# Kernel tuning notes

Hardware: AMD Instinct MI355X
Metric: run time of the kernel (lower is better)

The kernel has to match this reference:

```python
import jax, jax.numpy as jnp
import numpy as np

D_MODEL = 256
N_HEADS = 8


def setup_inputs() -> dict:
    key = jax.random.key(0)
    ks = jax.random.split(key, 12)
    B, S, d, H = 4, 1024, D_MODEL, N_HEADS
    s = 0.02
    return {
        "Q": jax.random.normal(ks[0], (B, S, d), jnp.float32),
        "K": jax.random.normal(ks[1], (B, S, d), jnp.float32),
        "V": jax.random.normal(ks[2], (B, S, d), jnp.float32),
        "Wq": jax.random.normal(ks[3], (d, d * H), jnp.float32) * s,
        "bq": jnp.zeros((d * H,), jnp.float32),
        "Wk": jax.random.normal(ks[4], (d, d * H), jnp.float32) * s,
        "bk": jnp.zeros((d * H,), jnp.float32),
        "Wv": jax.random.normal(ks[5], (d, d * H), jnp.float32) * s,
        "bv": jnp.zeros((d * H,), jnp.float32),
        "Wo": jax.random.normal(ks[6], (H * d, d), jnp.float32) * s,
        "bo": jnp.zeros((d,), jnp.float32),
    }


def reference(Q, K, V, Wq, bq, Wk, bk, Wv, bv, Wo, bo):
    B, S, d = Q.shape
    H = N_HEADS
    # projections: [B,S,d] -> [B,S,H*d] -> [B,H,S,d] (head_dim == d_model here)
    q = (Q @ Wq + bq).reshape(B, S, H, d).transpose(0, 2, 1, 3)
    k = (K @ Wk + bk).reshape(B, S, H, d).transpose(0, 2, 1, 3)
    v = (V @ Wv + bv).reshape(B, S, H, d).transpose(0, 2, 1, 3)
    scores = jnp.einsum("bhqd,bhkd->bhqk", q, k) / jnp.sqrt(jnp.float32(d))
    attn = jax.nn.softmax(scores, axis=-1)
    out = jnp.einsum("bhqk,bhkd->bhqd", attn, v)  # [B,H,S,d]
    out = out.transpose(0, 2, 1, 3).reshape(B, S, H * d)
    return out @ Wo + bo
```

## Files before the change

### kernel.cpp

```cpp
#include <hip/hip_runtime.h>
#include <stdint.h>

#define NB 4
#define SEQ 1024
#define DM 256
#define NH 8

typedef __attribute__((ext_vector_type(8))) short bf8;
typedef __attribute__((ext_vector_type(4))) float f4;

__device__ __forceinline__ unsigned short f2bf(float f) {
  union { float f; uint32_t u; } c; c.f = f;
  uint32_t u = c.u;
  return (unsigned short)((u + 0x7FFFu + ((u >> 16) & 1u)) >> 16);
}

__device__ __forceinline__ float bf2f(short s) {
  union { uint32_t u; float f; } c;
  c.u = ((uint32_t)(unsigned short)s) << 16;
  return c.f;
}

__device__ __forceinline__ void gl_lds16(const unsigned short* g, short* l) {
  __builtin_amdgcn_global_load_lds(
      (const __attribute__((address_space(1))) unsigned int*)g,
      (__attribute__((address_space(3))) unsigned int*)l, 16, 0, 0);
}


__global__ __launch_bounds__(256) void prep_kernel(
    const float* __restrict__ Wq, const float* __restrict__ Wk,
    const float* __restrict__ Wv, const float* __restrict__ Wo,
    const float* __restrict__ Q, const float* __restrict__ K,
    const float* __restrict__ V,
    unsigned short* __restrict__ Wt3, unsigned short* __restrict__ WoT,
    unsigned short* __restrict__ Xbf) {
  const int z = blockIdx.y;
  const int tid = threadIdx.x;
  if (z >= 4) {
    const float* src = (z == 4) ? Q : (z == 5) ? K : V;
    const size_t off = (size_t)blockIdx.x * 1024 + tid * 4;
    const float4 v = *(const float4*)(src + off);
    short4 s;
    s.x = (short)f2bf(v.x); s.y = (short)f2bf(v.y);
    s.z = (short)f2bf(v.z); s.w = (short)f2bf(v.w);
    *(short4*)(Xbf + (size_t)(z - 4) * 4096 * 256 + off) = s;
    return;
  }
  if (blockIdx.x >= 512) return;
  const float* in;
  unsigned short* out;
  int R, C, bx, by;
  if (z < 3) {
    in = (z == 0) ? Wq : (z == 1) ? Wk : Wv;
    out = Wt3 + (size_t)z * 2048 * 256;
    R = 256; C = 2048; bx = blockIdx.x & 63; by = blockIdx.x >> 6;
  } else {
    in = Wo; out = WoT;
    R = 2048; C = 256; bx = blockIdx.x & 7; by = blockIdx.x >> 3;
  }
  __shared__ float t[32][33];
  const int c0 = bx * 32, r0 = by * 32;
  const int tx = tid & 31, ty = tid >> 5;
#pragma unroll
  for (int i = 0; i < 4; i++) {
    int r = r0 + ty + i * 8;
    t[ty + i * 8][tx] = in[(size_t)r * C + c0 + tx];
  }
  __syncthreads();
#pragma unroll
  for (int i = 0; i < 4; i++) {
    int c = c0 + ty + i * 8;
    out[(size_t)c * R + r0 + tx] = f2bf(t[tx][ty + i * 8]);
  }
}

__global__ __launch_bounds__(256) void proj_kernel(
    const unsigned short* __restrict__ Xbf, const unsigned short* __restrict__ Wt3,
    const float* __restrict__ bq, const float* __restrict__ bk, const float* __restrict__ bv,
    unsigned short* __restrict__ q_frag, unsigned short* __restrict__ k_frag,
    unsigned short* __restrict__ v_frag) {
  const int z = blockIdx.z;
  const unsigned short* X = Xbf + (size_t)z * 4096 * 256;
  const unsigned short* Wt = Wt3 + (size_t)z * 2048 * 256;
  const float* bias = (z == 0) ? bq : (z == 1) ? bk : bv;

  __shared__ short a_lds[128 * 32];
  __shared__ short b_lds[128 * 32];

  const int tid = threadIdx.x;
  const int wid = tid >> 6, lane = tid & 63;
  const int quad = lane >> 4, l16 = lane & 15;
  const int wm = wid >> 1, wn = wid & 1;
  const int m0 = blockIdx.x * 128, n0 = blockIdx.y * 128;

  f4 acc[4][4];
  const f4 z4 = {0.f, 0.f, 0.f, 0.f};
#pragma unroll
  for (int i = 0; i < 4; i++)
#pragma unroll
    for (int j = 0; j < 4; j++) acc[i][j] = z4;

  const int srow = lane >> 2;
  const int schunk = lane & 3;
  const int cxor = quad ^ (l16 & 3);

  for (int ko = 0; ko < 8; ko++) {
    const int k0 = ko * 32;
#pragma unroll
    for (int j = 0; j < 2; j++) {
      const int i = wid * 2 + j;
      const int row = i * 16 + srow;
      const int sc = (schunk ^ (row & 3)) * 8;
      gl_lds16(X + (size_t)(m0 + row) * DM + k0 + sc, a_lds + i * 512);
      gl_lds16(Wt + (size_t)(n0 + row) * DM + k0 + sc, b_lds + i * 512);
    }
    __syncthreads();
    bf8 af[4], bfv[4];
#pragma unroll
    for (int mi = 0; mi < 4; mi++)
      af[mi] = *(const bf8*)(a_lds + (wm * 64 + mi * 16 + l16) * 32 + cxor * 8);
#pragma unroll
    for (int ni = 0; ni < 4; ni++)
      bfv[ni] = *(const bf8*)(b_lds + (wn * 64 + ni * 16 + l16) * 32 + cxor * 8);
    if (z < 2) {
#pragma unroll
      for (int ni = 0; ni < 4; ni++)
#pragma unroll
        for (int mi = 0; mi < 4; mi++)
          acc[ni][mi] = __builtin_amdgcn_mfma_f32_16x16x32_bf16(bfv[ni], af[mi], acc[ni][mi], 0, 0, 0);
    } else {
#pragma unroll
      for (int mi = 0; mi < 4; mi++)
#pragma unroll
        for (int ni = 0; ni < 4; ni++)
          acc[mi][ni] = __builtin_amdgcn_mfma_f32_16x16x32_bf16(af[mi], bfv[ni], acc[mi][ni], 0, 0, 0);
    }
    __syncthreads();
  }

  if (z < 2) {
    const float scale = (z == 0) ? 0.0901684400f : 1.0f;
    unsigned short* dst = (z == 0) ? q_frag : k_frag;
#pragma unroll
    for (int ni = 0; ni < 4; ni++) {
      const int nb = n0 + wn * 64 + ni * 16 + quad * 4;
      const float4 b4 = *(const float4*)(bias + nb);
      const int h = nb >> 8, dd = nb & 255;
      const int dq = (dd >> 3) & 3, jh = dd & 7;
#pragma unroll
      for (int mi = 0; mi < 4; mi++) {
        const int tok = m0 + wm * 64 + mi * 16 + l16;
        const int b = tok >> 10, sr = tok & 1023;
        const size_t idx = ((size_t)(b * NH + h) * 64 + (sr >> 4)) * 4096 +
                           (size_t)(dd >> 5) * 512 + ((sr & 15) + 16 * dq) * 8 + jh;
        short4 s4;
        s4.x = (short)f2bf((acc[ni][mi][0] + b4.x) * scale);
        s4.y = (short)f2bf((acc[ni][mi][1] + b4.y) * scale);
        s4.z = (short)f2bf((acc[ni][mi][2] + b4.z) * scale);
        s4.w = (short)f2bf((acc[ni][mi][3] + b4.w) * scale);
        *(short4*)(dst + idx) = s4;
      }
    }
  } else {
#pragma unroll
    for (int ni = 0; ni < 4; ni++) {
      const int n = n0 + wn * 64 + ni * 16 + l16;
      const float bsv = bias[n];
      const int h = n >> 8, d = n & 255;
#pragma unroll
      for (int mi = 0; mi < 4; mi++) {
        const int m = m0 + wm * 64 + mi * 16 + quad * 4;
        const int b = m >> 10, sr = m & 1023;
        const size_t idx = ((size_t)(b * NH + h) * 16 + (d >> 4)) * 16384 +
                           (size_t)(sr >> 5) * 512 +
                           ((d & 15) + 16 * ((sr >> 3) & 3)) * 8 + (sr & 7);
        short4 s4;
        s4.x = (short)f2bf(acc[mi][ni][0] + bsv);
        s4.y = (short)f2bf(acc[mi][ni][1] + bsv);
        s4.z = (short)f2bf(acc[mi][ni][2] + bsv);
        s4.w = (short)f2bf(acc[mi][ni][3] + bsv);
        *(short4*)(v_frag + idx) = s4;
      }
    }
  }
}

__global__ __launch_bounds__(256, 3) void attn_kernel(
    const unsigned short* __restrict__ q_frag, const unsigned short* __restrict__ k_frag,
    const unsigned short* __restrict__ v_frag, unsigned short* __restrict__ o_p0,
    unsigned short* __restrict__ o_p1, float* __restrict__ l_part, const int split) {
  __shared__ short k_lds[2][8192];
  __shared__ short p_lds[2][64][40];

  const int tid = threadIdx.x;
  const int wid = tid >> 6, lane = tid & 63;
  const int quad = lane >> 4, l16 = lane & 15;
  const int blk = blockIdx.x;
  const int g = blk & 7;
  const int qt = (blk >> 3) & 15;
  const int kvh = split ? ((blk >> 7) & 1) : 0;
  const int bh = g + 8 * (blk >> (split ? 8 : 7));
  const int t0 = kvh * 16;
  const int tlast = t0 + (split ? 15 : 31);
  const int nhalf = split ? 8 : 16;
  const size_t fbase = (size_t)bh * 262144;

  bf8 qf[8];
  {
    const unsigned short* qp = q_frag + fbase + (size_t)(qt * 4 + wid) * 4096 + lane * 8;
#pragma unroll
    for (int kc = 0; kc < 8; kc++) qf[kc] = *(const bf8*)(qp + kc * 512);
  }

  const f4 z4 = {0.f, 0.f, 0.f, 0.f};
  f4 Oacc[4][4];
#pragma unroll
  for (int i = 0; i < 4; i++)
#pragma unroll
    for (int j = 0; j < 4; j++) Oacc[i][j] = z4;
  float lpart[4] = {0.f, 0.f, 0.f, 0.f};

  const unsigned short* kdma_src = k_frag + fbase + (size_t)wid * 2048 + lane * 8;
#pragma unroll
  for (int jj = 0; jj < 4; jj++)
    gl_lds16(kdma_src + (size_t)t0 * 8192 + jj * 512, &k_lds[0][wid * 2048 + jj * 512]);
  __syncthreads();

  bf8 vpre0[4], vpre1[4];
  const unsigned short* vbase_p = v_frag + fbase + (size_t)(wid * 4) * 16384 + lane * 8;

#define ATTN_STEP(T, CUR, PRV, VCUR, VPRV)                                     \
  {                                                                            \
    const int t_ = (T);                                                        \
    _Pragma("unroll")                                                          \
    for (int mi = 0; mi < 4; mi++)                                             \
      VCUR[mi] = *(const bf8*)(vbase_p + (size_t)mi * 16384 + (size_t)t_ * 512); \
    f4 Sacc[2];                                                                \
    Sacc[0] = z4; Sacc[1] = z4;                                                \
    _Pragma("unroll")                                                          \
    for (int kc = 0; kc < 8; kc++) {                                           \
      const bf8 aq = qf[kc];                                                   \
      _Pragma("unroll")                                                        \
      for (int ni = 0; ni < 2; ni++) {                                         \
        const bf8 kb = *(const bf8*)(&k_lds[CUR][(ni * 8 + kc) * 512 + lane * 8]); \
        Sacc[ni] = __builtin_amdgcn_mfma_f32_16x16x32_bf16(aq, kb, Sacc[ni], 0, 0, 0); \
      }                                                                        \
    }                                                                          \
    if (t_ < tlast) {                                                          \
      _Pragma("unroll")                                                        \
      for (int jj = 0; jj < 4; jj++)                                           \
        gl_lds16(kdma_src + (size_t)(t_ + 1) * 8192 + jj * 512,                \
                 &k_lds[PRV][wid * 2048 + jj * 512]);                          \
    }                                                                          \
    if (t_ > t0) {                                                             \
      bf8 pb[4];                                                               \
      _Pragma("unroll")                                                        \
      for (int nq = 0; nq < 4; nq++)                                           \
        pb[nq] = *(const bf8*)(&p_lds[PRV][nq * 16 + l16][quad * 8]);          \
      _Pragma("unroll")                                                        \
      for (int mi = 0; mi < 4; mi++)                                           \
        _Pragma("unroll")                                                      \
        for (int nq = 0; nq < 4; nq++)                                         \
          Oacc[mi][nq] = __builtin_amdgcn_mfma_f32_16x16x32_bf16(VPRV[mi], pb[nq], Oacc[mi][nq], 0, 0, 0); \
    }                                                                          \
    _Pragma("unroll")                                                          \
    for (int reg = 0; reg < 4; reg++) {                                        \
      const int qrow = wid * 16 + quad * 4 + reg;                              \
      float s = 0.f;                                                           \
      _Pragma("unroll")                                                        \
      for (int ni = 0; ni < 2; ni++) {                                         \
        const float p = exp2f(Sacc[ni][reg]);                                  \
        s += p;                                                                \
        union { float f; uint32_t u; } c;                                      \
        c.f = p;                                                               \
        p_lds[CUR][qrow][ni * 16 + l16] = (short)((c.u + 0x8000u) >> 16);      \
      }                                                                        \
      lpart[reg] += s;                                                         \
    }                                                                          \
    __syncthreads();                                                           \
  }

  for (int tt = 0; tt < nhalf; tt++) {
    ATTN_STEP(t0 + tt * 2, 0, 1, vpre0, vpre1)
    ATTN_STEP(t0 + tt * 2 + 1, 1, 0, vpre1, vpre0)
  }
#undef ATTN_STEP

  {
    bf8 pb[4];
#pragma unroll
    for (int nq = 0; nq < 4; nq++)
      pb[nq] = *(const bf8*)(&p_lds[1][nq * 16 + l16][quad * 8]);
#pragma unroll
    for (int mi = 0; mi < 4; mi++)
#pragma unroll
      for (int nq = 0; nq < 4; nq++)
        Oacc[mi][nq] = __builtin_amdgcn_mfma_f32_16x16x32_bf16(vpre1[mi], pb[nq], Oacc[mi][nq], 0, 0, 0);
  }

#pragma unroll
  for (int reg = 0; reg < 4; reg++) {
    float v = lpart[reg];
    v += __shfl_xor(v, 1, 64);
    v += __shfl_xor(v, 2, 64);
    v += __shfl_xor(v, 4, 64);
    v += __shfl_xor(v, 8, 64);
    if (l16 == 0) {
      const size_t lidx = (size_t)bh * 1024 + qt * 64 + wid * 16 + quad * 4 + reg;
      l_part[(size_t)kvh * 32768 + lidx] = v;
      if (!split) l_part[32768 + lidx] = v;
    }
  }

  unsigned short* op = kvh ? o_p1 : o_p0;
  const int b = bh >> 3, h = bh & 7;
#pragma unroll
  for (int nq = 0; nq < 4; nq++) {
    const int q = nq * 16 + l16;
    const size_t base = ((size_t)b * SEQ + qt * 64 + q) * (NH * DM) + h * DM + wid * 64;
#pragma unroll
    for (int mi = 0; mi < 4; mi++) {
      short4 s4;
      s4.x = (short)f2bf(Oacc[mi][nq][0]);
      s4.y = (short)f2bf(Oacc[mi][nq][1]);
      s4.z = (short)f2bf(Oacc[mi][nq][2]);
      s4.w = (short)f2bf(Oacc[mi][nq][3]);
      *(short4*)(op + base + mi * 16 + quad * 4) = s4;
    }
  }
}

__global__ __launch_bounds__(256) void outproj_kernel(
    const unsigned short* __restrict__ o_p0, const unsigned short* __restrict__ o_p1,
    const float* __restrict__ l_part, const unsigned short* __restrict__ WoT,
    const float* __restrict__ bo, float* __restrict__ out) {
  __shared__ short a_lds[32][136];
  __shared__ short b_lds[64][136];

  const int tid = threadIdx.x;
  const int wid = tid >> 6, lane = tid & 63;
  const int quad = lane >> 4, l16 = lane & 15;
  const int wm = wid & 1, wn = wid >> 1;
  const int m0 = blockIdx.x * 32, n0 = blockIdx.y * 64;

  const f4 z4 = {0.f, 0.f, 0.f, 0.f};
  f4 acc[2];
#pragma unroll
  for (int i = 0; i < 2; i++) acc[i] = z4;

  const int ch = tid & 15, row = tid >> 4;
  for (int ko = 0; ko < 16; ko++) {
    const int k0 = ko * 128;
    const int h = k0 >> 8;
#pragma unroll
    for (int rb = 0; rb < 2; rb++) {
      const int r = row + rb * 16;
      const int token = m0 + r;
      const int b_ = token >> 10, sr = token & 1023;
      const size_t lidx = (size_t)(b_ * NH + h) * 1024 + sr;
      const float inv = 1.f / (l_part[lidx] + l_part[32768 + lidx]);
      const bf8 v0 = *(const bf8*)(o_p0 + (size_t)token * 2048 + k0 + ch * 8);
      const bf8 v1 = *(const bf8*)(o_p1 + (size_t)token * 2048 + k0 + ch * 8);
      bf8 s;
#pragma unroll
      for (int j = 0; j < 8; j++)
        s[j] = (short)f2bf((bf2f(v0[j]) + bf2f(v1[j])) * inv);
      *(bf8*)(&a_lds[r][ch * 8]) = s;
    }
#pragma unroll
    for (int rb = 0; rb < 4; rb++) {
      int r = row + rb * 16;
      *(bf8*)(&b_lds[r][ch * 8]) = *(const bf8*)(WoT + (size_t)(n0 + r) * 2048 + k0 + ch * 8);
    }
    __syncthreads();
#pragma unroll
    for (int kc = 0; kc < 4; kc++) {
      const bf8 af = *(const bf8*)(&a_lds[wm * 16 + l16][kc * 32 + quad * 8]);
      bf8 bfv[2];
#pragma unroll
      for (int ni = 0; ni < 2; ni++)
        bfv[ni] = *(const bf8*)(&b_lds[wn * 32 + ni * 16 + l16][kc * 32 + quad * 8]);
#pragma unroll
      for (int ni = 0; ni < 2; ni++)
        acc[ni] = __builtin_amdgcn_mfma_f32_16x16x32_bf16(af, bfv[ni], acc[ni], 0, 0, 0);
    }
    __syncthreads();
  }
#pragma unroll
  for (int ni = 0; ni < 2; ni++) {
    const int n = n0 + wn * 32 + ni * 16 + l16;
    const float bv = bo[n];
#pragma unroll
    for (int reg = 0; reg < 4; reg++) {
      const int m = m0 + wm * 16 + quad * 4 + reg;
      out[(size_t)m * DM + n] = acc[ni][reg] + bv;
    }
  }
}

extern "C" void kernel_launch(void* const* d_in, const int* in_sizes, int n_in,
                              void* d_out, int out_size, void* d_ws, size_t ws_size,
                              hipStream_t stream) {
  const float* Q  = (const float*)d_in[0];
  const float* K  = (const float*)d_in[1];
  const float* V  = (const float*)d_in[2];
  const float* Wq = (const float*)d_in[3];
  const float* bq = (const float*)d_in[4];
  const float* Wk = (const float*)d_in[5];
  const float* bk = (const float*)d_in[6];
  const float* Wv = (const float*)d_in[7];
  const float* bv = (const float*)d_in[8];
  const float* Wo = (const float*)d_in[9];
  const float* bo = (const float*)d_in[10];
  float* out = (float*)d_out;

  char* ws = (char*)d_ws;
  const size_t QS = (size_t)NB * NH * SEQ * DM * 2;
  const size_t WT = (size_t)2048 * 256 * 2;
  unsigned short* q_frag = (unsigned short*)(ws);
  unsigned short* k_frag = (unsigned short*)(ws + QS);
  unsigned short* v_frag = (unsigned short*)(ws + 2 * QS);
  unsigned short* o_p0   = (unsigned short*)(ws + 3 * QS);
  unsigned short* Wt3 = (unsigned short*)(ws + 4 * QS);
  unsigned short* WoT = (unsigned short*)(ws + 4 * QS + 3 * WT);
  float* l_part = (float*)(ws + 4 * QS);
  const size_t need_split = 4 * QS + 4 * WT + QS;
  const int split = (ws_size >= need_split) ? 1 : 0;
  unsigned short* o_p1 = split ? (unsigned short*)(ws + 4 * QS + 4 * WT) : o_p0;
  unsigned short* Xbf = o_p0;

  prep_kernel<<<dim3(1024, 7), 256, 0, stream>>>(Wq, Wk, Wv, Wo, Q, K, V,
                                                 Wt3, WoT, Xbf);
  proj_kernel<<<dim3(32, 16, 3), 256, 0, stream>>>(Xbf, Wt3, bq, bk, bv,
                                                   q_frag, k_frag, v_frag);
  attn_kernel<<<split ? 1024 : 512, 256, 0, stream>>>(q_frag, k_frag, v_frag,
                                                      o_p0, o_p1, l_part, split);
  outproj_kernel<<<dim3(128, 4), 256, 0, stream>>>(o_p0, o_p1, l_part, WoT, bo, out);
}
```

Before: 187.1 us.

## Merge prep work per block, deepen proj K-tile, single-buffer attention K tile

The prep kernel now launches 512 blocks, and each block loops over several conversion and transpose tiles instead of using a large 2D grid of mostly idle blocks. The projection GEMM now stages 64-wide K slices per barrier instead of 32, halving the number of sync rounds. The attention kernel drops the double-buffered K tile in LDS in favour of a single buffer: the next K load is issued after a barrier and a second barrier is added per step. The min-occupancy hint is removed from its launch bounds. Single buffering cuts LDS use to allow more resident blocks, at the cost of extra barriers and less overlap between the K load and the QK MFMAs.

```diff
diff --git a/kernel.cpp b/kernel.cpp
--- a/kernel.cpp
+++ b/kernel.cpp
@@ -26,7 +26,6 @@
       (const __attribute__((address_space(1))) unsigned int*)g,
       (__attribute__((address_space(3))) unsigned int*)l, 16, 0, 0);
 }
-
 
 __global__ __launch_bounds__(256) void prep_kernel(
     const float* __restrict__ Wq, const float* __restrict__ Wk,
@@ -35,43 +34,52 @@
     const float* __restrict__ V,
     unsigned short* __restrict__ Wt3, unsigned short* __restrict__ WoT,
     unsigned short* __restrict__ Xbf) {
-  const int z = blockIdx.y;
   const int tid = threadIdx.x;
-  if (z >= 4) {
-    const float* src = (z == 4) ? Q : (z == 5) ? K : V;
-    const size_t off = (size_t)blockIdx.x * 1024 + tid * 4;
-    const float4 v = *(const float4*)(src + off);
+  const int bid = blockIdx.x;
+
+#pragma unroll
+  for (int it = 0; it < 6; ++it) {
+    const int idx = (it * 512 + bid) * 256 + tid;
+    const int z = idx >> 18;
+    const int r = idx & 262143;
+    const float* src = (z == 0) ? Q : (z == 1) ? K : V;
+    const float4 v = *(const float4*)(src + (size_t)r * 4);
     short4 s;
     s.x = (short)f2bf(v.x); s.y = (short)f2bf(v.y);
     s.z = (short)f2bf(v.z); s.w = (short)f2bf(v.w);
-    *(short4*)(Xbf + (size_t)(z - 4) * 4096 * 256 + off) = s;
-    return;
-  }
-  if (blockIdx.x >= 512) return;
-  const float* in;
-  unsigned short* out;
-  int R, C, bx, by;
-  if (z < 3) {
-    in = (z == 0) ? Wq : (z == 1) ? Wk : Wv;
-    out = Wt3 + (size_t)z * 2048 * 256;
-    R = 256; C = 2048; bx = blockIdx.x & 63; by = blockIdx.x >> 6;
-  } else {
-    in = Wo; out = WoT;
-    R = 2048; C = 256; bx = blockIdx.x & 7; by = blockIdx.x >> 3;
-  }
+    *(short4*)(Xbf + (size_t)z * 1048576 + (size_t)r * 4) = s;
+  }
+
   __shared__ float t[32][33];
-  const int c0 = bx * 32, r0 = by * 32;
   const int tx = tid & 31, ty = tid >> 5;
-#pragma unroll
-  for (int i = 0; i < 4; i++) {
-    int r = r0 + ty + i * 8;
-    t[ty + i * 8][tx] = in[(size_t)r * C + c0 + tx];
-  }
-  __syncthreads();
-#pragma unroll
-  for (int i = 0; i < 4; i++) {
-    int c = c0 + ty + i * 8;
-    out[(size_t)c * R + r0 + tx] = f2bf(t[tx][ty + i * 8]);
+  for (int tt = 0; tt < 4; ++tt) {
+    const int id = bid * 4 + tt;
+    const float* in;
+    unsigned short* out;
+    int R, C, bx, by;
+    if (id < 1536) {
+      const int z = id >> 9, rem = id & 511;
+      in = (z == 0) ? Wq : (z == 1) ? Wk : Wv;
+      out = Wt3 + (size_t)z * 2048 * 256;
+      R = 256; C = 2048; bx = rem & 63; by = rem >> 6;
+    } else {
+      const int rem = id - 1536;
+      in = Wo; out = WoT;
+      R = 2048; C = 256; bx = rem & 7; by = rem >> 3;
+    }
+    const int c0 = bx * 32, r0 = by * 32;
+    __syncthreads();
+#pragma unroll
+    for (int i = 0; i < 4; i++) {
+      int r = r0 + ty + i * 8;
+      t[ty + i * 8][tx] = in[(size_t)r * C + c0 + tx];
+    }
+    __syncthreads();
+#pragma unroll
+    for (int i = 0; i < 4; i++) {
+      int c = c0 + ty + i * 8;
+      out[(size_t)c * R + r0 + tx] = f2bf(t[tx][ty + i * 8]);
+    }
   }
 }
 
@@ -85,8 +93,8 @@
   const unsigned short* Wt = Wt3 + (size_t)z * 2048 * 256;
   const float* bias = (z == 0) ? bq : (z == 1) ? bk : bv;
 
-  __shared__ short a_lds[128 * 32];
-  __shared__ short b_lds[128 * 32];
+  __shared__ short a_lds[128 * 64];
+  __shared__ short b_lds[128 * 64];
 
   const int tid = threadIdx.x;
   const int wid = tid >> 6, lane = tid & 63;
@@ -105,36 +113,40 @@
   const int schunk = lane & 3;
   const int cxor = quad ^ (l16 & 3);
 
-  for (int ko = 0; ko < 8; ko++) {
-    const int k0 = ko * 32;
-#pragma unroll
-    for (int j = 0; j < 2; j++) {
-      const int i = wid * 2 + j;
+  for (int ko = 0; ko < 4; ko++) {
+    const int k0 = ko * 64;
+#pragma unroll
+    for (int jj = 0; jj < 4; jj++) {
+      const int c = wid * 4 + jj;
+      const int kh = c >> 3, i = c & 7;
       const int row = i * 16 + srow;
       const int sc = (schunk ^ (row & 3)) * 8;
-      gl_lds16(X + (size_t)(m0 + row) * DM + k0 + sc, a_lds + i * 512);
-      gl_lds16(Wt + (size_t)(n0 + row) * DM + k0 + sc, b_lds + i * 512);
-    }
-    __syncthreads();
-    bf8 af[4], bfv[4];
-#pragma unroll
-    for (int mi = 0; mi < 4; mi++)
-      af[mi] = *(const bf8*)(a_lds + (wm * 64 + mi * 16 + l16) * 32 + cxor * 8);
-#pragma unroll
-    for (int ni = 0; ni < 4; ni++)
-      bfv[ni] = *(const bf8*)(b_lds + (wn * 64 + ni * 16 + l16) * 32 + cxor * 8);
-    if (z < 2) {
+      gl_lds16(X + (size_t)(m0 + row) * DM + k0 + kh * 32 + sc, a_lds + c * 512);
+      gl_lds16(Wt + (size_t)(n0 + row) * DM + k0 + kh * 32 + sc, b_lds + c * 512);
+    }
+    __syncthreads();
+#pragma unroll
+    for (int kh = 0; kh < 2; kh++) {
+      bf8 af[4], bfv[4];
+#pragma unroll
+      for (int mi = 0; mi < 4; mi++)
+        af[mi] = *(const bf8*)(a_lds + kh * 4096 + (wm * 64 + mi * 16 + l16) * 32 + cxor * 8);
 #pragma unroll
       for (int ni = 0; ni < 4; ni++)
+        bfv[ni] = *(const bf8*)(b_lds + kh * 4096 + (wn * 64 + ni * 16 + l16) * 32 + cxor * 8);
+      if (z < 2) {
+#pragma unroll
+        for (int ni = 0; ni < 4; ni++)
+#pragma unroll
+          for (int mi = 0; mi < 4; mi++)
+            acc[ni][mi] = __builtin_amdgcn_mfma_f32_16x16x32_bf16(bfv[ni], af[mi], acc[ni][mi], 0, 0, 0);
+      } else {
 #pragma unroll
         for (int mi = 0; mi < 4; mi++)
-          acc[ni][mi] = __builtin_amdgcn_mfma_f32_16x16x32_bf16(bfv[ni], af[mi], acc[ni][mi], 0, 0, 0);
-    } else {
-#pragma unroll
-      for (int mi = 0; mi < 4; mi++)
-#pragma unroll
-        for (int ni = 0; ni < 4; ni++)
-          acc[mi][ni] = __builtin_amdgcn_mfma_f32_16x16x32_bf16(af[mi], bfv[ni], acc[mi][ni], 0, 0, 0);
+#pragma unroll
+          for (int ni = 0; ni < 4; ni++)
+            acc[mi][ni] = __builtin_amdgcn_mfma_f32_16x16x32_bf16(af[mi], bfv[ni], acc[mi][ni], 0, 0, 0);
+      }
     }
     __syncthreads();
   }
@@ -186,11 +198,11 @@
   }
 }
 
-__global__ __launch_bounds__(256, 3) void attn_kernel(
+__global__ __launch_bounds__(256) void attn_kernel(
     const unsigned short* __restrict__ q_frag, const unsigned short* __restrict__ k_frag,
     const unsigned short* __restrict__ v_frag, unsigned short* __restrict__ o_p0,
     unsigned short* __restrict__ o_p1, float* __restrict__ l_part, const int split) {
-  __shared__ short k_lds[2][8192];
+  __shared__ short k_lds[8192];
   __shared__ short p_lds[2][64][40];
 
   const int tid = threadIdx.x;
@@ -224,7 +236,7 @@
   const unsigned short* kdma_src = k_frag + fbase + (size_t)wid * 2048 + lane * 8;
 #pragma unroll
   for (int jj = 0; jj < 4; jj++)
-    gl_lds16(kdma_src + (size_t)t0 * 8192 + jj * 512, &k_lds[0][wid * 2048 + jj * 512]);
+    gl_lds16(kdma_src + (size_t)t0 * 8192 + jj * 512, &k_lds[wid * 2048 + jj * 512]);
   __syncthreads();
 
   bf8 vpre0[4], vpre1[4];
@@ -243,26 +255,9 @@
       const bf8 aq = qf[kc];                                                   \
       _Pragma("unroll")                                                        \
       for (int ni = 0; ni < 2; ni++) {                                         \
-        const bf8 kb = *(const bf8*)(&k_lds[CUR][(ni * 8 + kc) * 512 + lane * 8]); \
+        const bf8 kb = *(const bf8*)(&k_lds[(ni * 8 + kc) * 512 + lane * 8]);  \
         Sacc[ni] = __builtin_amdgcn_mfma_f32_16x16x32_bf16(aq, kb, Sacc[ni], 0, 0, 0); \
       }                                                                        \
-    }                                                                          \
-    if (t_ < tlast) {                                                          \
-      _Pragma("unroll")                                                        \
-      for (int jj = 0; jj < 4; jj++)                                           \
-        gl_lds16(kdma_src + (size_t)(t_ + 1) * 8192 + jj * 512,                \
-                 &k_lds[PRV][wid * 2048 + jj * 512]);                          \
-    }                                                                          \
-    if (t_ > t0) {                                                             \
-      bf8 pb[4];                                                               \
-      _Pragma("unroll")                                                        \
-      for (int nq = 0; nq < 4; nq++)                                           \
-        pb[nq] = *(const bf8*)(&p_lds[PRV][nq * 16 + l16][quad * 8]);          \
-      _Pragma("unroll")                                                        \
-      for (int mi = 0; mi < 4; mi++)                                           \
-        _Pragma("unroll")                                                      \
-        for (int nq = 0; nq < 4; nq++)                                         \
-          Oacc[mi][nq] = __builtin_amdgcn_mfma_f32_16x16x32_bf16(VPRV[mi], pb[nq], Oacc[mi][nq], 0, 0, 0); \
     }                                                                          \
     _Pragma("unroll")                                                          \
     for (int reg = 0; reg < 4; reg++) {                                        \
@@ -278,7 +273,25 @@
       }                                                                        \
       lpart[reg] += s;                                                         \
     }                                                                          \
-    __syncthreads();                                                           \
+    __syncthreads();      \
+    if (t_ < tlast) {                                                          \
+      _Pragma("unroll")                                                        \
+      for (int jj = 0; jj < 4; jj++)                                           \
+        gl_lds16(kdma_src + (size_t)(t_ + 1) * 8192 + jj * 512,                \
+                 &k_lds[wid * 2048 + jj * 512]);                               \
+    }                                                                          \
+    if (t_ > t0) {                                                             \
+      bf8 pb[4];                                                               \
+      _Pragma("unroll")                                                        \
+      for (int nq = 0; nq < 4; nq++)                                           \
+        pb[nq] = *(const bf8*)(&p_lds[PRV][nq * 16 + l16][quad * 8]);          \
+      _Pragma("unroll")                                                        \
+      for (int mi = 0; mi < 4; mi++)                                           \
+        _Pragma("unroll")                                                      \
+        for (int nq = 0; nq < 4; nq++)                                         \
+          Oacc[mi][nq] = __builtin_amdgcn_mfma_f32_16x16x32_bf16(VPRV[mi], pb[nq], Oacc[mi][nq], 0, 0, 0); \
+    }                                                                          \
+    __syncthreads();                    \
   }
 
   for (int tt = 0; tt < nhalf; tt++) {
@@ -430,8 +443,8 @@
   unsigned short* o_p1 = split ? (unsigned short*)(ws + 4 * QS + 4 * WT) : o_p0;
   unsigned short* Xbf = o_p0;
 
-  prep_kernel<<<dim3(1024, 7), 256, 0, stream>>>(Wq, Wk, Wv, Wo, Q, K, V,
-                                                 Wt3, WoT, Xbf);
+  prep_kernel<<<512, 256, 0, stream>>>(Wq, Wk, Wv, Wo, Q, K, V,
+                                       Wt3, WoT, Xbf);
   proj_kernel<<<dim3(32, 16, 3), 256, 0, stream>>>(Xbf, Wt3, bq, bk, bv,
                                                    q_frag, k_frag, v_frag);
   attn_kernel<<<split ? 1024 : 512, 256, 0, stream>>>(q_frag, k_frag, v_frag,
```

Result: faster. 181.3 us (-3.1%).
